# Performance work log

Measured on AMD Instinct MI355X. Metric: run time of the kernel, lower is better.

## Reference

```python
import jax, jax.numpy as jnp
import numpy as np

N_NODES = 100000
EMB_DIM = 128
N_LAYERS = 3
N_EDGES = 1600000


def setup_inputs() -> dict:
    key = jax.random.key(0)
    ks = jax.random.split(key, 6)
    edge_index = jax.random.randint(ks[0], (2, N_EDGES), 0, N_NODES, dtype=jnp.int32)
    deg_inv = jax.random.uniform(ks[1], (N_NODES,), dtype=jnp.float32)
    node_emb = 0.02 * jax.random.normal(ks[2], (N_NODES, EMB_DIM), dtype=jnp.float32)
    W = jax.random.normal(ks[3], (N_LAYERS, EMB_DIM, EMB_DIM), dtype=jnp.float32) / np.sqrt(EMB_DIM)
    b = jnp.zeros((N_LAYERS, EMB_DIM), dtype=jnp.float32)
    gamma = jnp.ones((EMB_DIM,), dtype=jnp.float32)
    beta = jnp.zeros((EMB_DIM,), dtype=jnp.float32)
    return {"edge_index": edge_index, "deg_inv": deg_inv, "node_emb": node_emb,
            "W": W, "b": b, "gamma": gamma, "beta": beta}


def reference(edge_index, deg_inv, node_emb, W, b, gamma, beta):
    src, dst = edge_index[0], edge_index[1]
    x = node_emb  # [N, d]
    for l in range(N_LAYERS):
        # scatter-add neighbor aggregation: m[v] = sum_{(u->v)} x[u]
        m = jax.ops.segment_sum(x[src], dst, num_segments=N_NODES)  # [N, d]
        m = m * deg_inv[:, None]
        h = jax.nn.gelu(m @ W[l] + b[l], approximate=False)  # dropout=0 (eval)
        x = x + h  # residual
    # LayerNorm over feature dim
    mu = jnp.mean(x, axis=-1, keepdims=True)
    var = jnp.var(x, axis=-1, keepdims=True)
    x = (x - mu) * jax.lax.rsqrt(var + 1e-5) * gamma + beta
    return x
```

## Files before the change

kernel.cpp:

```cpp
#include <hip/hip_runtime.h>
#include <hip/hip_bf16.h>
#include <math.h>

#define N_NODES 100000
#define EMB 128
#define N_EDGES 1600000
#define N_LAYERS 3

#define NB 400
#define NPB 250
#define CAP 8192
#define CAPB 6144
#define BSTR 16
#define EPT 8
#define BUCKET_THREADS 512
#define BUCKET_BLOCKS ((N_EDGES + BUCKET_THREADS * EPT - 1) / (BUCKET_THREADS * EPT))

typedef __bf16 bf16x8 __attribute__((ext_vector_type(8)));
typedef float f32x4 __attribute__((ext_vector_type(4)));


__global__ __launch_bounds__(BUCKET_THREADS) void bucket_kernel(
    const int* __restrict__ src, const int* __restrict__ dst,
    int* __restrict__ bcur, unsigned* __restrict__ pairs) {
  __shared__ int scnt[NB];
  __shared__ int sbase[NB];
  const int t = threadIdx.x;
  if (t < NB) scnt[t] = 0;
  __syncthreads();
  unsigned pk[EPT];
  int bk[EPT], lofs[EPT];
  const int base_e = blockIdx.x * BUCKET_THREADS * EPT;
#pragma unroll
  for (int it = 0; it < EPT; ++it) {
    int i = base_e + it * BUCKET_THREADS + t;
    bk[it] = -1;
    if (i < N_EDGES) {
      int d = dst[i];
      int s = src[i];
      int b = d / NPB;
      int vloc = d - b * NPB;
      bk[it] = b;
      pk[it] = ((unsigned)vloc << 17) | (unsigned)s;
      lofs[it] = atomicAdd(&scnt[b], 1);
    }
  }
  __syncthreads();
  if (t < NB) sbase[t] = atomicAdd(&bcur[t * BSTR], scnt[t]);
  __syncthreads();
#pragma unroll
  for (int it = 0; it < EPT; ++it) {
    if (bk[it] >= 0) {
      int idx = sbase[bk[it]] + lofs[it];
      if (idx < CAP) pairs[(size_t)bk[it] * CAP + idx] = pk[it];
    }
  }
}

__device__ __forceinline__ int* scan512(int* pin, int* pout, int t) {
  for (int off = 1; off < 512; off <<= 1) {
    for (int i = t; i < 512; i += 256) {
      int v = pin[i];
      if (i >= off) v += pin[i - off];
      pout[i] = v;
    }
    __syncthreads();
    int* tmp = pin; pin = pout; pout = tmp;
  }
  return pin;
}

__global__ __launch_bounds__(256) void fillb_kernel(const unsigned* __restrict__ pairs,
                                                    const int* __restrict__ bcur,
                                                    int* __restrict__ row_ptr,
                                                    int* __restrict__ col) {
  __shared__ int sA[512], sB[512];
  __shared__ int cnt[NPB], cur[NPB];
  __shared__ unsigned pstage[CAPB];
  __shared__ int colstage[CAPB];
  const int t = threadIdx.x;
  const int b = blockIdx.x;

  for (int i = t; i < 512; i += 256) sA[i] = (i < NB) ? bcur[i * BSTR] : 0;
  __syncthreads();
  int* r = scan512(sA, sB, t);
  int base_b = b ? r[b - 1] : 0;
  int n = r[b] - base_b;
  if (n > CAP) n = CAP;
  const unsigned* pg = pairs + (size_t)b * CAP;
  const bool fits = (n <= CAPB);

  if (fits) for (int i = t; i < n; i += 256) pstage[i] = pg[i];
  if (t < NPB) cnt[t] = 0;
  __syncthreads();
  for (int i = t; i < n; i += 256) atomicAdd(&cnt[(fits ? pstage[i] : pg[i]) >> 17], 1);
  __syncthreads();
  for (int i = t; i < 512; i += 256) sA[i] = (i < NPB) ? cnt[i] : 0;
  __syncthreads();
  r = scan512(sA, sB, t);
  if (t < NPB) {
    int ex = r[t] - cnt[t];
    row_ptr[b * NPB + t] = base_b + ex;
    cur[t] = ex;
  }
  if (b == NB - 1 && t == 0) row_ptr[N_NODES] = N_EDGES;
  __syncthreads();
  for (int i = t; i < n; i += 256) {
    unsigned p = fits ? pstage[i] : pg[i];
    int pos = atomicAdd(&cur[p >> 17], 1);
    int s = (int)(p & 0x1FFFFu);
    if (fits) colstage[pos] = s;
    else col[base_b + pos] = s;
  }
  __syncthreads();
  if (fits) for (int i = t; i < n; i += 256) col[base_b + i] = colstage[i];
}


__global__ __launch_bounds__(256) void tobf16_kernel(const float* __restrict__ in,
                                                     __hip_bfloat16* __restrict__ xb) {
  size_t i = (size_t)blockIdx.x * 256 + threadIdx.x;
  const float4* p = (const float4*)in + i * 2;
  float4 a = p[0], b = p[1];
  union { __hip_bfloat16 h[8]; uint4 u; } r;
  r.h[0] = __float2bfloat16(a.x); r.h[1] = __float2bfloat16(a.y);
  r.h[2] = __float2bfloat16(a.z); r.h[3] = __float2bfloat16(a.w);
  r.h[4] = __float2bfloat16(b.x); r.h[5] = __float2bfloat16(b.y);
  r.h[6] = __float2bfloat16(b.z); r.h[7] = __float2bfloat16(b.w);
  ((uint4*)xb)[i] = r.u;
}

__global__ __launch_bounds__(256) void wt_kernel(const float* __restrict__ W,
                                                 __hip_bfloat16* __restrict__ WT) {
  int l = blockIdx.x;
  const float* Wl = W + (size_t)l * EMB * EMB;
  __hip_bfloat16* WTl = WT + (size_t)l * EMB * EMB;
  for (int i = threadIdx.x; i < EMB * EMB; i += 256) {
    int k = i >> 7, c = i & 127;
    WTl[c * EMB + k] = __float2bfloat16(Wl[i]);
  }
}


__device__ __forceinline__ float bf_lo(unsigned int w) { return __uint_as_float(w << 16); }
__device__ __forceinline__ float bf_hi(unsigned int w) { return __uint_as_float(w & 0xFFFF0000u); }

__device__ __forceinline__ float gelu_exact(float v) {
  return 0.5f * v * (1.f + erff(v * 0.70710678118654752f));
}

template <int LAST>
__global__ __launch_bounds__(512, 8) void fused_kernel(
    const __hip_bfloat16* __restrict__ xb_in,
    const int* __restrict__ row_ptr,
    const int* __restrict__ col,
    const float* __restrict__ deg_inv,
    const __hip_bfloat16* __restrict__ WTl,
    const float* __restrict__ bias,
    __hip_bfloat16* __restrict__ xb_out,
    float* __restrict__ xf_out,
    const float* __restrict__ gamma,
    const float* __restrict__ beta) {
  __shared__ __hip_bfloat16 sM[16][136];

  const int t = threadIdx.x;
  const int w = t >> 6;
  const int lane = t & 63;
  const int q = lane >> 4;
  const int l15 = lane & 15;
  const int row0b = blockIdx.x * 16;

  const char* gbase = (const char*)xb_in + l15 * 16;
  for (int nn = 0; nn < 2; ++nn) {
    const int v = __builtin_amdgcn_readfirstlane(row0b + w * 2 + nn);
    const int beg = row_ptr[v], end = row_ptr[v + 1];
    float a0 = 0.f, a1 = 0.f, a2 = 0.f, a3 = 0.f, a4 = 0.f, a5 = 0.f, a6 = 0.f, a7 = 0.f;
#define ACC8(W) { a0 += bf_lo(W.x); a1 += bf_hi(W.x); a2 += bf_lo(W.y); a3 += bf_hi(W.y); \
                  a4 += bf_lo(W.z); a5 += bf_hi(W.z); a6 += bf_lo(W.w); a7 += bf_hi(W.w); }
    int e = beg;
    for (; e + 16 <= end; e += 16) {
      int u0 = col[e + q];
      int u1 = col[e + 4 + q];
      int u2 = col[e + 8 + q];
      int u3 = col[e + 12 + q];
      uint4 w0 = *(const uint4*)(gbase + (size_t)u0 * 256);
      uint4 w1 = *(const uint4*)(gbase + (size_t)u1 * 256);
      uint4 w2 = *(const uint4*)(gbase + (size_t)u2 * 256);
      uint4 w3 = *(const uint4*)(gbase + (size_t)u3 * 256);
      ACC8(w0) ACC8(w1) ACC8(w2) ACC8(w3)
    }
    for (; e < end; e += 4) {
      int idx = e + q;
      bool valid = idx < end;
      int u = col[valid ? idx : beg];
      uint4 w0 = *(const uint4*)(gbase + (size_t)u * 256);
      if (valid) ACC8(w0)
    }
#undef ACC8
    a0 += __shfl_xor(a0, 16, 64); a0 += __shfl_xor(a0, 32, 64);
    a1 += __shfl_xor(a1, 16, 64); a1 += __shfl_xor(a1, 32, 64);
    a2 += __shfl_xor(a2, 16, 64); a2 += __shfl_xor(a2, 32, 64);
    a3 += __shfl_xor(a3, 16, 64); a3 += __shfl_xor(a3, 32, 64);
    a4 += __shfl_xor(a4, 16, 64); a4 += __shfl_xor(a4, 32, 64);
    a5 += __shfl_xor(a5, 16, 64); a5 += __shfl_xor(a5, 32, 64);
    a6 += __shfl_xor(a6, 16, 64); a6 += __shfl_xor(a6, 32, 64);
    a7 += __shfl_xor(a7, 16, 64); a7 += __shfl_xor(a7, 32, 64);
    if (q == 0) {
      float di = deg_inv[v];
      union { __hip_bfloat16 h[8]; uint4 u4; } r;
      r.h[0] = __float2bfloat16(a0 * di); r.h[1] = __float2bfloat16(a1 * di);
      r.h[2] = __float2bfloat16(a2 * di); r.h[3] = __float2bfloat16(a3 * di);
      r.h[4] = __float2bfloat16(a4 * di); r.h[5] = __float2bfloat16(a5 * di);
      r.h[6] = __float2bfloat16(a6 * di); r.h[7] = __float2bfloat16(a7 * di);
      *(uint4*)(&sM[w * 2 + nn][l15 * 8]) = r.u4;
    }
  }

  bf16x8 bfr[4];
  {
    const __hip_bfloat16* wp = WTl + (size_t)(w * 16 + l15) * EMB + q * 8;
#pragma unroll
    for (int ks = 0; ks < 4; ++ks)
      bfr[ks] = *(const bf16x8*)(wp + ks * 32);
  }
  __syncthreads();

  f32x4 acc = (f32x4)(0.f);
#pragma unroll
  for (int ks = 0; ks < 4; ++ks) {
    bf16x8 af = *(const bf16x8*)(&sM[l15][q * 8 + ks * 32]);
    acc = __builtin_amdgcn_mfma_f32_16x16x32_bf16(af, bfr[ks], acc, 0, 0, 0);
  }
  __syncthreads();
  {
    const int colg = w * 16 + l15;
    const float bb = bias[colg];
#pragma unroll
    for (int j = 0; j < 4; ++j)
      sM[q * 4 + j][colg] = __float2bfloat16(gelu_exact(acc[j] + bb));
  }
  __syncthreads();

#pragma unroll
  for (int rr = 0; rr < 2; ++rr) {
    const int r = w * 2 + rr;
    const size_t rowoff = (size_t)(row0b + r) * EMB;
    unsigned rg = *(const unsigned*)(&sM[r][lane * 2]);
    unsigned rd = *(const unsigned*)((const char*)xb_in + (rowoff + lane * 2) * 2);
    float v1 = bf_lo(rd) + bf_lo(rg);
    float v2 = bf_hi(rd) + bf_hi(rg);
    if (!LAST) {
      union { __hip_bfloat16 h[2]; unsigned u; } o;
      o.h[0] = __float2bfloat16(v1);
      o.h[1] = __float2bfloat16(v2);
      *(unsigned*)((char*)xb_out + (rowoff + lane * 2) * 2) = o.u;
    } else {
      float s = v1 + v2;
      float sq = fmaf(v1, v1, v2 * v2);
      for (int off = 1; off < 64; off <<= 1) {
        s += __shfl_xor(s, off, 64);
        sq += __shfl_xor(sq, off, 64);
      }
      float mu = s * (1.f / EMB);
      float var = sq * (1.f / EMB) - mu * mu;
      float rstd = rsqrtf(var + 1e-5f);
      float2 g = *(const float2*)(gamma + lane * 2);
      float2 be = *(const float2*)(beta + lane * 2);
      float2 o;
      o.x = (v1 - mu) * rstd * g.x + be.x;
      o.y = (v2 - mu) * rstd * g.y + be.y;
      *(float2*)(xf_out + rowoff + lane * 2) = o;
    }
  }
}


extern "C" void kernel_launch(void* const* d_in, const int* in_sizes, int n_in,
                              void* d_out, int out_size, void* d_ws, size_t ws_size,
                              hipStream_t stream) {
  const int* edge_index = (const int*)d_in[0];
  const float* deg_inv = (const float*)d_in[1];
  const float* node_emb = (const float*)d_in[2];
  const float* W = (const float*)d_in[3];
  const float* b = (const float*)d_in[4];
  const float* gamma = (const float*)d_in[5];
  const float* beta = (const float*)d_in[6];
  const int* src = edge_index;
  const int* dst = edge_index + N_EDGES;
  float* x = (float*)d_out;

  char* ws = (char*)d_ws;
  auto take = [&](size_t bytes) {
    char* p = ws;
    ws += (bytes + 255) & ~(size_t)255;
    return p;
  };
  __hip_bfloat16* xbA = (__hip_bfloat16*)take((size_t)N_NODES * EMB * 2);
  __hip_bfloat16* xbB = (__hip_bfloat16*)take((size_t)N_NODES * EMB * 2);
  __hip_bfloat16* WT = (__hip_bfloat16*)take((size_t)N_LAYERS * EMB * EMB * 2);
  int* row_ptr = (int*)take((N_NODES + 1) * sizeof(int));
  int* col = (int*)take(N_EDGES * sizeof(int));
  int* bcur = (int*)take(NB * BSTR * sizeof(int));
  unsigned* pairs = (unsigned*)xbB;

  hipMemsetAsync(bcur, 0, NB * BSTR * sizeof(int), stream);

  tobf16_kernel<<<N_NODES * EMB / 8 / 256, 256, 0, stream>>>(node_emb, xbA);
  wt_kernel<<<N_LAYERS, 256, 0, stream>>>(W, WT);

  bucket_kernel<<<BUCKET_BLOCKS, BUCKET_THREADS, 0, stream>>>(src, dst, bcur, pairs);
  fillb_kernel<<<NB, 256, 0, stream>>>(pairs, bcur, row_ptr, col);

  const int NBLK = N_NODES / 16;
  fused_kernel<0><<<NBLK, 512, 0, stream>>>(xbA, row_ptr, col, deg_inv,
                                            WT, b, xbB, nullptr, nullptr, nullptr);
  fused_kernel<0><<<NBLK, 512, 0, stream>>>(xbB, row_ptr, col, deg_inv,
                                            WT + (size_t)EMB * EMB, b + EMB,
                                            xbA, nullptr, nullptr, nullptr);
  fused_kernel<1><<<NBLK, 512, 0, stream>>>(xbA, row_ptr, col, deg_inv,
                                            WT + (size_t)2 * EMB * EMB, b + 2 * EMB,
                                            nullptr, x, gamma, beta);
}
```

Before: 301.3 us.

## Gather neighbor rows one per wave with dword loads; merge prep kernels

Each wave now aggregates one neighbor row per loop step, with every lane loading 4 bytes (two bf16 values), instead of four rows at once with 16-byte loads per lane. This removes the cross-quarter shuffle reduction, and the column indices become wave-uniform. A separate shared-memory buffer for GELU output removes one barrier, and the residual row loads are issued before the barrier. The two prep kernels are merged into one launch. The trade-off is narrower loads per lane and fewer independent gathers in flight per iteration, which could reduce memory-level parallelism.

```diff
diff --git a/kernel.cpp b/kernel.cpp
--- a/kernel.cpp
+++ b/kernel.cpp
@@ -117,27 +117,28 @@
 }
 
 
-__global__ __launch_bounds__(256) void tobf16_kernel(const float* __restrict__ in,
-                                                     __hip_bfloat16* __restrict__ xb) {
-  size_t i = (size_t)blockIdx.x * 256 + threadIdx.x;
-  const float4* p = (const float4*)in + i * 2;
-  float4 a = p[0], b = p[1];
-  union { __hip_bfloat16 h[8]; uint4 u; } r;
-  r.h[0] = __float2bfloat16(a.x); r.h[1] = __float2bfloat16(a.y);
-  r.h[2] = __float2bfloat16(a.z); r.h[3] = __float2bfloat16(a.w);
-  r.h[4] = __float2bfloat16(b.x); r.h[5] = __float2bfloat16(b.y);
-  r.h[6] = __float2bfloat16(b.z); r.h[7] = __float2bfloat16(b.w);
-  ((uint4*)xb)[i] = r.u;
-}
-
-__global__ __launch_bounds__(256) void wt_kernel(const float* __restrict__ W,
-                                                 __hip_bfloat16* __restrict__ WT) {
-  int l = blockIdx.x;
-  const float* Wl = W + (size_t)l * EMB * EMB;
-  __hip_bfloat16* WTl = WT + (size_t)l * EMB * EMB;
-  for (int i = threadIdx.x; i < EMB * EMB; i += 256) {
-    int k = i >> 7, c = i & 127;
-    WTl[c * EMB + k] = __float2bfloat16(Wl[i]);
+__global__ __launch_bounds__(256) void prep_kernel(const float* __restrict__ in,
+                                                   __hip_bfloat16* __restrict__ xb,
+                                                   const float* __restrict__ W,
+                                                   __hip_bfloat16* __restrict__ WT) {
+  if (blockIdx.x < N_NODES * EMB / 8 / 256) {
+    size_t i = (size_t)blockIdx.x * 256 + threadIdx.x;
+    const float4* p = (const float4*)in + i * 2;
+    float4 a = p[0], b = p[1];
+    union { __hip_bfloat16 h[8]; uint4 u; } r;
+    r.h[0] = __float2bfloat16(a.x); r.h[1] = __float2bfloat16(a.y);
+    r.h[2] = __float2bfloat16(a.z); r.h[3] = __float2bfloat16(a.w);
+    r.h[4] = __float2bfloat16(b.x); r.h[5] = __float2bfloat16(b.y);
+    r.h[6] = __float2bfloat16(b.z); r.h[7] = __float2bfloat16(b.w);
+    ((uint4*)xb)[i] = r.u;
+  } else {
+    int l = blockIdx.x - N_NODES * EMB / 8 / 256;
+    const float* Wl = W + (size_t)l * EMB * EMB;
+    __hip_bfloat16* WTl = WT + (size_t)l * EMB * EMB;
+    for (int i = threadIdx.x; i < EMB * EMB; i += 256) {
+      int k = i >> 7, c = i & 127;
+      WTl[c * EMB + k] = __float2bfloat16(Wl[i]);
+    }
   }
 }
 
@@ -162,6 +163,7 @@
     const float* __restrict__ gamma,
     const float* __restrict__ beta) {
   __shared__ __hip_bfloat16 sM[16][136];
+  __shared__ __hip_bfloat16 sG[16][136];
 
   const int t = threadIdx.x;
   const int w = t >> 6;
@@ -170,50 +172,31 @@
   const int l15 = lane & 15;
   const int row0b = blockIdx.x * 16;
 
-  const char* gbase = (const char*)xb_in + l15 * 16;
+  const char* gbase = (const char*)xb_in + lane * 4;
   for (int nn = 0; nn < 2; ++nn) {
     const int v = __builtin_amdgcn_readfirstlane(row0b + w * 2 + nn);
     const int beg = row_ptr[v], end = row_ptr[v + 1];
-    float a0 = 0.f, a1 = 0.f, a2 = 0.f, a3 = 0.f, a4 = 0.f, a5 = 0.f, a6 = 0.f, a7 = 0.f;
-#define ACC8(W) { a0 += bf_lo(W.x); a1 += bf_hi(W.x); a2 += bf_lo(W.y); a3 += bf_hi(W.y); \
-                  a4 += bf_lo(W.z); a5 += bf_hi(W.z); a6 += bf_lo(W.w); a7 += bf_hi(W.w); }
+    float ax = 0.f, ay = 0.f;
     int e = beg;
-    for (; e + 16 <= end; e += 16) {
-      int u0 = col[e + q];
-      int u1 = col[e + 4 + q];
-      int u2 = col[e + 8 + q];
-      int u3 = col[e + 12 + q];
-      uint4 w0 = *(const uint4*)(gbase + (size_t)u0 * 256);
-      uint4 w1 = *(const uint4*)(gbase + (size_t)u1 * 256);
-      uint4 w2 = *(const uint4*)(gbase + (size_t)u2 * 256);
-      uint4 w3 = *(const uint4*)(gbase + (size_t)u3 * 256);
-      ACC8(w0) ACC8(w1) ACC8(w2) ACC8(w3)
-    }
-    for (; e < end; e += 4) {
-      int idx = e + q;
-      bool valid = idx < end;
-      int u = col[valid ? idx : beg];
-      uint4 w0 = *(const uint4*)(gbase + (size_t)u * 256);
-      if (valid) ACC8(w0)
-    }
-#undef ACC8
-    a0 += __shfl_xor(a0, 16, 64); a0 += __shfl_xor(a0, 32, 64);
-    a1 += __shfl_xor(a1, 16, 64); a1 += __shfl_xor(a1, 32, 64);
-    a2 += __shfl_xor(a2, 16, 64); a2 += __shfl_xor(a2, 32, 64);
-    a3 += __shfl_xor(a3, 16, 64); a3 += __shfl_xor(a3, 32, 64);
-    a4 += __shfl_xor(a4, 16, 64); a4 += __shfl_xor(a4, 32, 64);
-    a5 += __shfl_xor(a5, 16, 64); a5 += __shfl_xor(a5, 32, 64);
-    a6 += __shfl_xor(a6, 16, 64); a6 += __shfl_xor(a6, 32, 64);
-    a7 += __shfl_xor(a7, 16, 64); a7 += __shfl_xor(a7, 32, 64);
-    if (q == 0) {
-      float di = deg_inv[v];
-      union { __hip_bfloat16 h[8]; uint4 u4; } r;
-      r.h[0] = __float2bfloat16(a0 * di); r.h[1] = __float2bfloat16(a1 * di);
-      r.h[2] = __float2bfloat16(a2 * di); r.h[3] = __float2bfloat16(a3 * di);
-      r.h[4] = __float2bfloat16(a4 * di); r.h[5] = __float2bfloat16(a5 * di);
-      r.h[6] = __float2bfloat16(a6 * di); r.h[7] = __float2bfloat16(a7 * di);
-      *(uint4*)(&sM[w * 2 + nn][l15 * 8]) = r.u4;
-    }
+    for (; e + 4 <= end; e += 4) {
+      int u0 = col[e], u1 = col[e + 1], u2 = col[e + 2], u3 = col[e + 3];
+      unsigned w0 = *(const unsigned*)(gbase + (size_t)u0 * 256);
+      unsigned w1 = *(const unsigned*)(gbase + (size_t)u1 * 256);
+      unsigned w2 = *(const unsigned*)(gbase + (size_t)u2 * 256);
+      unsigned w3 = *(const unsigned*)(gbase + (size_t)u3 * 256);
+      ax += bf_lo(w0) + bf_lo(w1) + bf_lo(w2) + bf_lo(w3);
+      ay += bf_hi(w0) + bf_hi(w1) + bf_hi(w2) + bf_hi(w3);
+    }
+    for (; e < end; ++e) {
+      unsigned w0 = *(const unsigned*)(gbase + (size_t)col[e] * 256);
+      ax += bf_lo(w0);
+      ay += bf_hi(w0);
+    }
+    float di = deg_inv[v];
+    union { __hip_bfloat16 h[2]; unsigned u; } r;
+    r.h[0] = __float2bfloat16(ax * di);
+    r.h[1] = __float2bfloat16(ay * di);
+    *(unsigned*)(&sM[w * 2 + nn][lane * 2]) = r.u;
   }
 
   bf16x8 bfr[4];
@@ -223,6 +206,10 @@
     for (int ks = 0; ks < 4; ++ks)
       bfr[ks] = *(const bf16x8*)(wp + ks * 32);
   }
+  unsigned rd0 = *(const unsigned*)((const char*)xb_in +
+                                    ((size_t)(row0b + w * 2) * EMB + lane * 2) * 2);
+  unsigned rd1 = *(const unsigned*)((const char*)xb_in +
+                                    ((size_t)(row0b + w * 2 + 1) * EMB + lane * 2) * 2);
   __syncthreads();
 
   f32x4 acc = (f32x4)(0.f);
@@ -231,13 +218,12 @@
     bf16x8 af = *(const bf16x8*)(&sM[l15][q * 8 + ks * 32]);
     acc = __builtin_amdgcn_mfma_f32_16x16x32_bf16(af, bfr[ks], acc, 0, 0, 0);
   }
-  __syncthreads();
   {
     const int colg = w * 16 + l15;
     const float bb = bias[colg];
 #pragma unroll
     for (int j = 0; j < 4; ++j)
-      sM[q * 4 + j][colg] = __float2bfloat16(gelu_exact(acc[j] + bb));
+      sG[q * 4 + j][colg] = __float2bfloat16(gelu_exact(acc[j] + bb));
   }
   __syncthreads();
 
@@ -245,8 +231,8 @@
   for (int rr = 0; rr < 2; ++rr) {
     const int r = w * 2 + rr;
     const size_t rowoff = (size_t)(row0b + r) * EMB;
-    unsigned rg = *(const unsigned*)(&sM[r][lane * 2]);
-    unsigned rd = *(const unsigned*)((const char*)xb_in + (rowoff + lane * 2) * 2);
+    unsigned rg = *(const unsigned*)(&sG[r][lane * 2]);
+    unsigned rd = rr ? rd1 : rd0;
     float v1 = bf_lo(rd) + bf_lo(rg);
     float v2 = bf_hi(rd) + bf_hi(rg);
     if (!LAST) {
@@ -305,8 +291,7 @@
 
   hipMemsetAsync(bcur, 0, NB * BSTR * sizeof(int), stream);
 
-  tobf16_kernel<<<N_NODES * EMB / 8 / 256, 256, 0, stream>>>(node_emb, xbA);
-  wt_kernel<<<N_LAYERS, 256, 0, stream>>>(W, WT);
+  prep_kernel<<<N_NODES * EMB / 8 / 256 + N_LAYERS, 256, 0, stream>>>(node_emb, xbA, W, WT);
 
   bucket_kernel<<<BUCKET_BLOCKS, BUCKET_THREADS, 0, stream>>>(src, dst, bcur, pairs);
   fillb_kernel<<<NB, 256, 0, stream>>>(pairs, bcur, row_ptr, col);
```

Measured after the change: 293.1 us, median of 2. 1.03x faster.
